# Kernel optimization log

Measured on AMD Instinct MI355X. Metric: run time of the kernel, lower is better.

The kernel has to match this reference:

```python
import jax, jax.numpy as jnp
import numpy as np
import math

B, S, D = 4, 1024, 1024
H, DK = 16, 64
NUM_BUCKETS = 32
MAX_DISTANCE = 128


def _relative_position_bucket(relative_position, bidirectional=True,
                              num_buckets=32, max_distance=128):
    # faithful port of T5's bucketing
    relative_buckets = jnp.zeros_like(relative_position)
    if bidirectional:
        num_buckets //= 2
        relative_buckets = relative_buckets + (relative_position > 0).astype(jnp.int32) * num_buckets
        relative_position = jnp.abs(relative_position)
    else:
        relative_position = -jnp.minimum(relative_position, jnp.zeros_like(relative_position))
    max_exact = num_buckets // 2
    is_small = relative_position < max_exact
    rp_safe = jnp.maximum(relative_position, 1)  # avoid log(0); masked by is_small
    rel_if_large = max_exact + (
        jnp.log(rp_safe.astype(jnp.float32) / max_exact)
        / math.log(max_distance / max_exact) * (num_buckets - max_exact)
    ).astype(jnp.int32)
    rel_if_large = jnp.minimum(rel_if_large, num_buckets - 1)
    return relative_buckets + jnp.where(is_small, relative_position, rel_if_large)


def compute_bias(rel_bias_emb, query_length, key_length):
    ctx = jnp.arange(query_length, dtype=jnp.int32)[:, None]
    mem = jnp.arange(key_length, dtype=jnp.int32)[None, :]
    rp = mem - ctx  # [q, k]
    buckets = _relative_position_bucket(rp, bidirectional=True,
                                        num_buckets=NUM_BUCKETS,
                                        max_distance=MAX_DISTANCE)
    values = rel_bias_emb[buckets]          # [q, k, h]
    return jnp.transpose(values, (2, 0, 1))[None]  # [1, h, q, k]


def setup_inputs() -> dict:
    key = jax.random.key(0)
    ks = jax.random.split(key, 6)
    s = 1.0 / math.sqrt(D)
    return {
        "hidden_states": jax.random.normal(ks[0], (B, S, D), jnp.float32),
        "Wq": jax.random.normal(ks[1], (D, H * DK), jnp.float32) * s,
        "Wk": jax.random.normal(ks[2], (D, H * DK), jnp.float32) * s,
        "Wv": jax.random.normal(ks[3], (D, H * DK), jnp.float32) * s,
        "Wo": jax.random.normal(ks[4], (H * DK, D), jnp.float32) * s,
        "rel_bias_emb": jax.random.normal(ks[5], (NUM_BUCKETS, H), jnp.float32),
    }


def reference(hidden_states, Wq, Wk, Wv, Wo, rel_bias_emb):
    b, s, _ = hidden_states.shape

    def shape_heads(x):  # [b, s, h*dk] -> [b, h, s, dk]
        return x.reshape(b, s, H, DK).transpose(0, 2, 1, 3)

    q = shape_heads(hidden_states @ Wq)
    k = shape_heads(hidden_states @ Wk)
    v = shape_heads(hidden_states @ Wv)

    # T5 attention: no 1/sqrt(dk) scaling
    scores = jnp.einsum('bhqd,bhkd->bhqk', q, k)
    position_bias = compute_bias(rel_bias_emb, s, s)  # [1, h, s, s]
    scores = scores + position_bias
    attn = jax.nn.softmax(scores.astype(jnp.float32), axis=-1).astype(scores.dtype)
    ctx = jnp.einsum('bhqk,bhkd->bhqd', attn, v)
    ctx = ctx.transpose(0, 2, 1, 3).reshape(b, s, H * DK)
    return ctx @ Wo
```

## Files before the change

### kernel.cpp

```cpp
#include <hip/hip_runtime.h>

typedef unsigned short u16;
typedef unsigned int u32;
typedef __bf16 bf16x8 __attribute__((ext_vector_type(8)));
typedef float f32x4 __attribute__((ext_vector_type(4)));

#define MFMA16(a, b, c) __builtin_amdgcn_mfma_f32_16x16x32_bf16(a, b, c, 0, 0, 0)
#define LOG2E 1.4426950408889634f

__device__ __forceinline__ u16 f2bf(float f) {
  u32 u = __float_as_uint(f);
  u += 0x7FFFu + ((u >> 16) & 1u);
  return (u16)(u >> 16);
}

__device__ __forceinline__ void gld16(u16* lds, const u16* g) {
  __builtin_amdgcn_global_load_lds((const __attribute__((address_space(1))) void*)g,
                                   (__attribute__((address_space(3))) void*)lds,
                                   16, 0, 0);
}

__device__ __forceinline__ int t5_bucket(int rp) {
  int ret = rp > 0 ? 16 : 0;
  int a = rp < 0 ? -rp : rp;
  int b;
  if      (a <  8) b = a;
  else if (a < 12) b = 8;
  else if (a < 16) b = 9;
  else if (a < 23) b = 10;
  else if (a < 32) b = 11;
  else if (a < 46) b = 12;
  else if (a < 64) b = 13;
  else if (a < 91) b = 14;
  else             b = 15;
  return ret + b;
}

__global__ __launch_bounds__(256) void prep(const float4* __restrict__ X, ushort4* __restrict__ Xb,
                                            const float* __restrict__ w0, const float* __restrict__ w1,
                                            const float* __restrict__ w2, const float* __restrict__ w3,
                                            u16* __restrict__ out) {
  int bid = blockIdx.x;
  if (bid < 512) {
#pragma unroll
    for (int i = 0; i < 8; i++) {
      int g = bid * 2048 + i * 256 + threadIdx.x;
      float4 v = X[g];
      ushort4 o;
      o.x = f2bf(v.x); o.y = f2bf(v.y); o.z = f2bf(v.z); o.w = f2bf(v.w);
      Xb[g] = o;
    }
    return;
  }
  bid -= 512;
  __shared__ __align__(16) u16 tb[64 * 68];
  const int col = threadIdx.x & 63;
  const int rowo = threadIdx.x >> 6;
#pragma unroll 1
  for (int t2 = 0; t2 < 2; t2++) {
    const int tile = bid * 2 + t2;
    const int z = tile >> 8, t = tile & 255;
    const float* W = (z == 0) ? w0 : (z == 1) ? w1 : (z == 2) ? w2 : w3;
    u16* O = out + z * 1048576;
    const int n0 = (t & 15) * 64, k0 = (t >> 4) * 64;
#pragma unroll
    for (int r = 0; r < 16; r++) {
      int kl = r * 4 + rowo;
      tb[col * 68 + kl] = f2bf(W[(k0 + kl) * 1024 + n0 + col]);
    }
    __syncthreads();
#pragma unroll
    for (int r = 0; r < 16; r++) {
      int nl = r * 4 + rowo;
      O[(n0 + nl) * 1024 + k0 + col] = tb[nl * 68 + col];
    }
    __syncthreads();
  }
}

__global__ __launch_bounds__(256) void gemm128(const u16* __restrict__ A,
                                               const u16* __restrict__ BtBase,
                                               u16* __restrict__ outp) {
  __shared__ __align__(16) u16 smem[24576];
  const int tid = threadIdx.x, lane = tid & 63, wave = tid >> 6;
  const int l15 = lane & 15, quad = lane >> 4;
  const int wm = (wave >> 1) * 64, wn = (wave & 1) * 64;

  const int id = blockIdx.x + blockIdx.y * 24;
  const int xcd = id & 7, jj = id >> 3;
  const int nz = (jj % 12) + (xcd & 1) * 12;
  const int ymb = (jj / 12) + (xcd >> 1) * 8;
  const int n = nz / 3, z = nz % 3;
  const int m0 = ymb * 128, n0 = n * 128;
  const u16* Ab = A + m0 * 1024;
  const u16* Bb = BtBase + z * 1048576 + n0 * 1024;

  int cc0 = tid, cc1 = 256 + tid;
  int row0 = cc0 >> 2, row1 = cc1 >> 2;
  int aoff0 = row0 * 1024 + (((cc0 & 3) ^ ((row0 >> 1) & 3)) * 8);
  int aoff1 = row1 * 1024 + (((cc1 & 3) ^ ((row1 >> 1) & 3)) * 8);

  f32x4 acc[4][4];
  const f32x4 vz = {0.f, 0.f, 0.f, 0.f};
#pragma unroll
  for (int i = 0; i < 4; i++)
#pragma unroll
    for (int j = 0; j < 4; j++) acc[i][j] = vz;

  const int sk = (l15 >> 1) & 3;

  {
    gld16(smem + cc0 * 8, Ab + aoff0);
    gld16(smem + cc1 * 8, Ab + aoff1);
    gld16(smem + 4096 + cc0 * 8, Bb + aoff0);
    gld16(smem + 4096 + cc1 * 8, Bb + aoff1);
    gld16(smem + 8192 + cc0 * 8, Ab + 32 + aoff0);
    gld16(smem + 8192 + cc1 * 8, Ab + 32 + aoff1);
    gld16(smem + 12288 + cc0 * 8, Bb + 32 + aoff0);
    gld16(smem + 12288 + cc1 * 8, Bb + 32 + aoff1);
  }

  int cs = 0, ls = 2;
#pragma unroll 1
  for (int kt = 0; kt < 32; kt++) {
    if (kt < 30) {
      u16* dst = smem + ls * 8192;
      const int ka = (kt + 2) * 32;
      gld16(dst + cc0 * 8, Ab + ka + aoff0);
      gld16(dst + cc1 * 8, Ab + ka + aoff1);
      gld16(dst + 4096 + cc0 * 8, Bb + ka + aoff0);
      gld16(dst + 4096 + cc1 * 8, Bb + ka + aoff1);
      asm volatile("s_waitcnt vmcnt(8)\n\ts_barrier" ::: "memory");
    } else if (kt == 30) {
      asm volatile("s_waitcnt vmcnt(4)\n\ts_barrier" ::: "memory");
    } else {
      asm volatile("s_waitcnt vmcnt(0)\n\ts_barrier" ::: "memory");
    }
    u16* st = smem + cs * 8192;
    bf16x8 af[4], bg[4];
#pragma unroll
    for (int mt = 0; mt < 4; mt++)
      af[mt] = *(const bf16x8*)(st + (wm + mt * 16 + l15) * 32 + ((quad ^ sk) * 8));
#pragma unroll
    for (int nt = 0; nt < 4; nt++)
      bg[nt] = *(const bf16x8*)(st + 4096 + (wn + nt * 16 + l15) * 32 + ((quad ^ sk) * 8));
#pragma unroll
    for (int mt = 0; mt < 4; mt++)
#pragma unroll
      for (int nt = 0; nt < 4; nt++)
        acc[mt][nt] = MFMA16(af[mt], bg[nt], acc[mt][nt]);
    asm volatile("s_barrier" ::: "memory");
    cs = (cs == 2) ? 0 : cs + 1;
    ls = (ls == 2) ? 0 : ls + 1;
  }
  __syncthreads();

  if (z == 2) {
    u16* O = outp + z * 4194304;
#pragma unroll
    for (int mt = 0; mt < 4; mt++)
#pragma unroll
      for (int nt = 0; nt < 4; nt++) {
        int col = wn + nt * 16 + l15;
        int rowb = wm + mt * 16 + quad * 4;
        uint2 p;
        p.x = (u32)f2bf(acc[mt][nt][0]) | ((u32)f2bf(acc[mt][nt][1]) << 16);
        p.y = (u32)f2bf(acc[mt][nt][2]) | ((u32)f2bf(acc[mt][nt][3]) << 16);
        *(uint2*)(smem + col * 136 + rowb) = p;
      }
    __syncthreads();
    const int b = m0 >> 10, sbase = m0 & 1023;
#pragma unroll
    for (int p = 0; p < 8; p++) {
      int g = p * 256 + tid;
      int col = g >> 4, chunk = g & 15;
      uint4 v = *(const uint4*)(smem + col * 136 + chunk * 8);
      int nn = n0 + col, hh = nn >> 6, dk = nn & 63;
      *(uint4*)(O + ((b * 16 + hh) * 64 + dk) * 1024 + sbase + chunk * 8) = v;
    }
  } else {
    u16* O = outp + z * 4194304;
    const float scl = (z == 0) ? LOG2E : 1.0f;
#pragma unroll
    for (int mt = 0; mt < 4; mt++)
#pragma unroll
      for (int nt = 0; nt < 4; nt++) {
        int rowb = wm + mt * 16 + quad * 4;
        int colb = wn + nt * 16 + l15;
#pragma unroll
        for (int reg = 0; reg < 4; reg++)
          smem[(rowb + reg) * 144 + colb] = f2bf(acc[mt][nt][reg] * scl);
      }
    __syncthreads();
    const int b = m0 >> 10, sbase = m0 & 1023;
#pragma unroll
    for (int p = 0; p < 8; p++) {
      int g = p * 256 + tid;
      int ml = g >> 4, c = g & 15;
      uint4 v = *(const uint4*)(smem + ml * 144 + c * 8);
      int nn = n0 + c * 8, hh = nn >> 6, dk = nn & 63;
      *(uint4*)(O + (b * 16 + hh) * 65536 + (sbase + ml) * 64 + dk) = v;
    }
  }
}

__global__ __launch_bounds__(256) void attn(const u16* __restrict__ Q, const u16* __restrict__ K,
                                            const u16* __restrict__ V, const float* __restrict__ emb,
                                            u16* __restrict__ ctx) {
  __shared__ __align__(16) u16 sKV[2 * 8192];
  __shared__ __align__(16) u16 sP[128 * 72];
  __shared__ __align__(16) float4 bt4[1156];
  const int tid = threadIdx.x, lane = tid & 63, wave = tid >> 6;
  const int l15 = lane & 15, quad = lane >> 4;
  const int bh = blockIdx.x, qt = blockIdx.y;
  const int h = bh & 15, b = bh >> 4;
  const u16* Qp = Q + bh * 65536 + qt * 8192;
  const u16* Kp = K + bh * 65536;
  const u16* Vp = V + bh * 65536;
  const int sx = l15 & 7;

  int koff[2], voff[2], cbs[2];
#pragma unroll
  for (int r = 0; r < 2; r++) {
    int cb = r * 256 + wave * 64;
    int cc = cb + lane;
    int row = cc >> 3, c8 = (cc & 7) ^ (row & 7);
    koff[r] = row * 64 + c8 * 8;
    voff[r] = row * 1024 + c8 * 8;
    cbs[r] = cb * 8;
  }

  bf16x8 aq[2][2];
#pragma unroll
  for (int u = 0; u < 2; u++)
#pragma unroll
    for (int kk = 0; kk < 2; kk++)
      aq[u][kk] = *(const bf16x8*)(Qp + (wave * 32 + u * 16 + l15) * 64 + kk * 32 + quad * 8);

#pragma unroll
  for (int r = 0; r < 2; r++) {
    gld16(sKV + cbs[r], Kp + koff[r]);
    gld16(sKV + 4096 + cbs[r], Vp + voff[r]);
  }

  for (int i = tid; i < 1156; i += 256) {
    int rp0 = i - 127 - qt * 128;
    float4 v;
    v.x = emb[t5_bucket(rp0)     * 16 + h] * LOG2E;
    v.y = emb[t5_bucket(rp0 + 1) * 16 + h] * LOG2E;
    v.z = emb[t5_bucket(rp0 + 2) * 16 + h] * LOG2E;
    v.w = emb[t5_bucket(rp0 + 3) * 16 + h] * LOG2E;
    bt4[i] = v;
  }
  const float bias_pos = emb[31 * 16 + h] * LOG2E;
  const float bias_neg = emb[15 * 16 + h] * LOG2E;

  float2 ls2[2] = {{0.f, 0.f}, {0.f, 0.f}};
  f32x4 oc[2][4];
  const f32x4 vzero = {0.f, 0.f, 0.f, 0.f};
#pragma unroll
  for (int u = 0; u < 2; u++)
#pragma unroll
    for (int nt = 0; nt < 4; nt++) oc[u][nt] = vzero;

  __syncthreads();

#pragma unroll 1
  for (int j = 0; j < 16; j++) {
    u16* st = sKV + (j & 1) * 8192;
    if (j < 15) {
      u16* dst = sKV + ((j + 1) & 1) * 8192;
      const u16* Kj1 = Kp + (j + 1) * 4096;
      const u16* Vj1 = Vp + (j + 1) * 64;
#pragma unroll
      for (int r = 0; r < 2; r++) {
        gld16(dst + cbs[r], Kj1 + koff[r]);
        gld16(dst + 4096 + cbs[r], Vj1 + voff[r]);
      }
      asm volatile("s_waitcnt vmcnt(4)\n\ts_barrier" ::: "memory");
    } else {
      asm volatile("s_waitcnt vmcnt(0)\n\ts_barrier" ::: "memory");
    }

    f32x4 sc[4][2];
    const int rp_min = j * 64 - qt * 128 - 127;
    const int rp_max = j * 64 + 63 - qt * 128;
    if (rp_min >= 91) {
#pragma unroll
      for (int mt = 0; mt < 4; mt++)
#pragma unroll
        for (int u = 0; u < 2; u++) { sc[mt][u][0] = bias_pos; sc[mt][u][1] = bias_pos; sc[mt][u][2] = bias_pos; sc[mt][u][3] = bias_pos; }
    } else if (rp_max <= -91) {
#pragma unroll
      for (int mt = 0; mt < 4; mt++)
#pragma unroll
        for (int u = 0; u < 2; u++) { sc[mt][u][0] = bias_neg; sc[mt][u][1] = bias_neg; sc[mt][u][2] = bias_neg; sc[mt][u][3] = bias_neg; }
    } else {
#pragma unroll
      for (int mt = 0; mt < 4; mt++)
#pragma unroll
        for (int u = 0; u < 2; u++) {
          int idx = j * 64 + mt * 16 + quad * 4 - wave * 32 - u * 16 - l15 + 127;
          float4 bv4 = bt4[idx];
          sc[mt][u][0] = bv4.x; sc[mt][u][1] = bv4.y; sc[mt][u][2] = bv4.z; sc[mt][u][3] = bv4.w;
        }
    }
#pragma unroll
    for (int kk = 0; kk < 2; kk++) {
      bf16x8 ak[4];
      int g8 = kk * 4 + quad;
#pragma unroll
      for (int mt = 0; mt < 4; mt++)
        ak[mt] = *(const bf16x8*)(st + (mt * 16 + l15) * 64 + (g8 ^ sx) * 8);
#pragma unroll
      for (int mt = 0; mt < 4; mt++)
#pragma unroll
        for (int u = 0; u < 2; u++)
          sc[mt][u] = MFMA16(ak[mt], aq[u][kk], sc[mt][u]);
    }

#pragma unroll
    for (int u = 0; u < 2; u++) {
      const int prow = wave * 32 + u * 16 + l15;
#pragma unroll
      for (int mt = 0; mt < 4; mt++) {
        u32 b0 = __float_as_uint(__builtin_amdgcn_exp2f(sc[mt][u][0]));
        u32 b1 = __float_as_uint(__builtin_amdgcn_exp2f(sc[mt][u][1]));
        u32 b2 = __float_as_uint(__builtin_amdgcn_exp2f(sc[mt][u][2]));
        u32 b3 = __float_as_uint(__builtin_amdgcn_exp2f(sc[mt][u][3]));
        u32 t0 = b0 & 0xFFFF0000u, t1 = b1 & 0xFFFF0000u;
        u32 t2 = b2 & 0xFFFF0000u, t3 = b3 & 0xFFFF0000u;
        ls2[u].x += __uint_as_float(t0) + __uint_as_float(t2);
        ls2[u].y += __uint_as_float(t1) + __uint_as_float(t3);
        uint2 pk;
        pk.x = (t0 >> 16) | t1;
        pk.y = (t2 >> 16) | t3;
        *(uint2*)(sP + prow * 72 + mt * 16 + quad * 4) = pk;
      }
    }
    asm volatile("s_waitcnt lgkmcnt(0)" ::: "memory");

#pragma unroll
    for (int kk = 0; kk < 2; kk++) {
      bf16x8 ap[2];
      int g8 = kk * 4 + quad;
#pragma unroll
      for (int u = 0; u < 2; u++)
        ap[u] = *(const bf16x8*)(sP + (wave * 32 + u * 16 + l15) * 72 + kk * 32 + quad * 8);
#pragma unroll
      for (int nt = 0; nt < 4; nt++) {
        bf16x8 bv = *(const bf16x8*)(st + 4096 + (nt * 16 + l15) * 64 + (g8 ^ sx) * 8);
#pragma unroll
        for (int u = 0; u < 2; u++)
          oc[u][nt] = MFMA16(ap[u], bv, oc[u][nt]);
      }
    }
    asm volatile("s_barrier" ::: "memory");
  }

  float lsum[2];
#pragma unroll
  for (int u = 0; u < 2; u++) {
    lsum[u] = ls2[u].x + ls2[u].y;
    lsum[u] += __shfl_xor(lsum[u], 16, 64);
    lsum[u] += __shfl_xor(lsum[u], 32, 64);
  }
  float linv[2][4];
#pragma unroll
  for (int u = 0; u < 2; u++)
#pragma unroll
    for (int reg = 0; reg < 4; reg++)
      linv[u][reg] = __builtin_amdgcn_rcpf(__shfl(lsum[u], quad * 4 + reg, 64));

  u16* cb2 = ctx + b * 1048576 + (qt * 128 + wave * 32) * 1024 + h * 64;
#pragma unroll
  for (int u = 0; u < 2; u++)
#pragma unroll
    for (int nt = 0; nt < 4; nt++)
#pragma unroll
      for (int reg = 0; reg < 4; reg++)
        cb2[(u * 16 + quad * 4 + reg) * 1024 + nt * 16 + l15] = f2bf(oc[u][nt][reg] * linv[u][reg]);
}

__global__ __launch_bounds__(256) void gemm_o(const u16* __restrict__ A,
                                              const u16* __restrict__ Bt,
                                              float* __restrict__ O) {
  __shared__ __align__(16) u16 smem[36864];
  const int tid = threadIdx.x, lane = tid & 63, wave = tid >> 6;
  const int l15 = lane & 15, quad = lane >> 4;
  const int m0 = blockIdx.x * 64, n0 = blockIdx.y * 128;
  const u16* Ab = A + m0 * 1024;
  const u16* Bb = Bt + n0 * 1024;
  const int wn = wave * 32;

  int ar0 = tid >> 3, ar1 = (256 + tid) >> 3;
  int aoff0 = ar0 * 1024 + (((tid & 7) ^ (ar0 & 7)) * 8);
  int aoff1 = ar1 * 1024 + ((((256 + tid) & 7) ^ (ar1 & 7)) * 8);
  int boff[4], bdst[4];
#pragma unroll
  for (int r = 0; r < 4; r++) {
    int cc = r * 256 + tid;
    int row = cc >> 3;
    boff[r] = row * 1024 + (((cc & 7) ^ (row & 7)) * 8);
    bdst[r] = cc * 8;
  }

  f32x4 acc[4][2];
  const f32x4 vz = {0.f, 0.f, 0.f, 0.f};
#pragma unroll
  for (int i = 0; i < 4; i++) { acc[i][0] = vz; acc[i][1] = vz; }

  const int sx = l15 & 7;

#pragma unroll
  for (int s = 0; s < 2; s++) {
    u16* st = smem + s * 12288;
    const int ka = s * 64;
    gld16(st + tid * 8, Ab + ka + aoff0);
    gld16(st + (256 + tid) * 8, Ab + ka + aoff1);
#pragma unroll
    for (int r = 0; r < 4; r++) gld16(st + 4096 + bdst[r], Bb + ka + boff[r]);
  }

  int cs = 0, ls = 2;
#pragma unroll 1
  for (int kt = 0; kt < 16; kt++) {
    if (kt < 14) {
      u16* dst = smem + ls * 12288;
      const int ka = (kt + 2) * 64;
      gld16(dst + tid * 8, Ab + ka + aoff0);
      gld16(dst + (256 + tid) * 8, Ab + ka + aoff1);
#pragma unroll
      for (int r = 0; r < 4; r++) gld16(dst + 4096 + bdst[r], Bb + ka + boff[r]);
      asm volatile("s_waitcnt vmcnt(12)\n\ts_barrier" ::: "memory");
    } else if (kt == 14) {
      asm volatile("s_waitcnt vmcnt(6)\n\ts_barrier" ::: "memory");
    } else {
      asm volatile("s_waitcnt vmcnt(0)\n\ts_barrier" ::: "memory");
    }
    u16* st = smem + cs * 12288;
#pragma unroll
    for (int kk = 0; kk < 2; kk++) {
      bf16x8 af[4], bg[2];
      int g8 = kk * 4 + quad;
#pragma unroll
      for (int mt = 0; mt < 4; mt++)
        af[mt] = *(const bf16x8*)(st + (mt * 16 + l15) * 64 + ((g8 ^ sx) * 8));
#pragma unroll
      for (int nt = 0; nt < 2; nt++)
        bg[nt] = *(const bf16x8*)(st + 4096 + (wn + nt * 16 + l15) * 64 + ((g8 ^ sx) * 8));
#pragma unroll
      for (int mt = 0; mt < 4; mt++)
#pragma unroll
        for (int nt = 0; nt < 2; nt++)
          acc[mt][nt] = MFMA16(af[mt], bg[nt], acc[mt][nt]);
    }
    asm volatile("s_barrier" ::: "memory");
    cs = (cs == 2) ? 0 : cs + 1;
    ls = (ls == 2) ? 0 : ls + 1;
  }

#pragma unroll
  for (int mt = 0; mt < 4; mt++)
#pragma unroll
    for (int nt = 0; nt < 2; nt++)
#pragma unroll
      for (int reg = 0; reg < 4; reg++) {
        int row = m0 + mt * 16 + quad * 4 + reg;
        int col = n0 + wn + nt * 16 + l15;
        O[row * 1024 + col] = acc[mt][nt][reg];
      }
}

extern "C" void kernel_launch(void* const* d_in, const int* in_sizes, int n_in,
                              void* d_out, int out_size, void* d_ws, size_t ws_size,
                              hipStream_t stream) {
  (void)in_sizes; (void)n_in; (void)out_size; (void)ws_size;
  const float* X   = (const float*)d_in[0];
  const float* Wq  = (const float*)d_in[1];
  const float* Wk  = (const float*)d_in[2];
  const float* Wv  = (const float*)d_in[3];
  const float* Wo  = (const float*)d_in[4];
  const float* emb = (const float*)d_in[5];

  char* ws = (char*)d_ws;
  u16* Xb  = (u16*)(ws);
  u16* Wt  = (u16*)(ws + (8u  << 20));
  u16* Qb  = (u16*)(ws + (16u << 20));
  u16* Ctx = (u16*)(ws + (40u << 20));

  prep<<<1024, 256, 0, stream>>>((const float4*)X, (ushort4*)Xb, Wq, Wk, Wv, Wo, Wt);
  gemm128<<<dim3(24, 32), 256, 0, stream>>>(Xb, Wt, Qb);
  attn<<<dim3(64, 8), 256, 0, stream>>>(Qb, Qb + 4194304, Qb + 2 * 4194304, emb, Ctx);
  gemm_o<<<dim3(64, 8), 256, 0, stream>>>(Ctx, Wt + 3 * 1048576, (float*)d_out);
}
```

Baseline: 163.7 us.

## Split QKV projection into 128x256 Q/K kernel and separate V GEMM, enlarge output-GEMM tile

Replaces the single fused QKV GEMM (128x128 tiles with an XCD-aware remap) with a 512-thread kernel that computes Q and K using 128x256 tiles, plus a separate GEMM for V that keeps its transposed store. The output projection moves from 64x128 to 128x128 tiles with four 64x64 waves, so operand tiles are reused more per block. In exchange it adds a kernel launch, drops the XCD grouping, and lowers block counts, which reduces occupancy and parallelism on a 256-CU device.

After: 172.5 us. +5.4%, slower.

```diff
diff --git a/kernel.cpp b/kernel.cpp
--- a/kernel.cpp
+++ b/kernel.cpp
@@ -78,22 +78,120 @@
   }
 }
 
-__global__ __launch_bounds__(256) void gemm128(const u16* __restrict__ A,
-                                               const u16* __restrict__ BtBase,
-                                               u16* __restrict__ outp) {
+__global__ __launch_bounds__(512) void qk512(const u16* __restrict__ A,
+                                             const u16* __restrict__ Wt,
+                                             u16* __restrict__ outp) {
+  __shared__ __align__(16) u16 smem[36864];
+  const int tid = threadIdx.x, lane = tid & 63, wave = tid >> 6;
+  const int l15 = lane & 15, quad = (lane >> 4) & 3;
+  const int wm = (wave >> 2) * 64, wn = (wave & 3) * 64;
+  const int id = blockIdx.x;
+  const int nq = id & 7, m = id >> 3;
+  const int m0 = m * 128, n0 = nq * 256;
+  const int z = nq >> 2;
+  const u16* Ab = A + m0 * 1024;
+  const u16* Bb = Wt + n0 * 1024;
+
+  const int ar = tid >> 2;
+  const int aoff = ar * 1024 + (((tid & 3) ^ ((ar >> 1) & 3)) * 8);
+  int boff[2], bdst[2];
+#pragma unroll
+  for (int r = 0; r < 2; r++) {
+    int cc = r * 512 + tid;
+    int row = cc >> 2;
+    boff[r] = row * 1024 + (((cc & 3) ^ ((row >> 1) & 3)) * 8);
+    bdst[r] = 4096 + cc * 8;
+  }
+
+  f32x4 acc[4][4];
+  const f32x4 vz = {0.f, 0.f, 0.f, 0.f};
+#pragma unroll
+  for (int i = 0; i < 4; i++)
+#pragma unroll
+    for (int j = 0; j < 4; j++) acc[i][j] = vz;
+
+  const int sk = (l15 >> 1) & 3;
+
+#pragma unroll
+  for (int s = 0; s < 2; s++) {
+    u16* st = smem + s * 12288;
+    const int ka = s * 32;
+    gld16(st + tid * 8, Ab + ka + aoff);
+    gld16(st + bdst[0], Bb + ka + boff[0]);
+    gld16(st + bdst[1], Bb + ka + boff[1]);
+  }
+
+  int cs = 0, ls = 2;
+#pragma unroll 1
+  for (int kt = 0; kt < 32; kt++) {
+    if (kt < 30) {
+      u16* dst = smem + ls * 12288;
+      const int ka = (kt + 2) * 32;
+      gld16(dst + tid * 8, Ab + ka + aoff);
+      gld16(dst + bdst[0], Bb + ka + boff[0]);
+      gld16(dst + bdst[1], Bb + ka + boff[1]);
+      asm volatile("s_waitcnt vmcnt(6)\n\ts_barrier" ::: "memory");
+    } else if (kt == 30) {
+      asm volatile("s_waitcnt vmcnt(3)\n\ts_barrier" ::: "memory");
+    } else {
+      asm volatile("s_waitcnt vmcnt(0)\n\ts_barrier" ::: "memory");
+    }
+    u16* st = smem + cs * 12288;
+    bf16x8 af[4], bg[4];
+#pragma unroll
+    for (int mt = 0; mt < 4; mt++)
+      af[mt] = *(const bf16x8*)(st + (wm + mt * 16 + l15) * 32 + ((quad ^ sk) * 8));
+#pragma unroll
+    for (int nt = 0; nt < 4; nt++)
+      bg[nt] = *(const bf16x8*)(st + 4096 + (wn + nt * 16 + l15) * 32 + ((quad ^ sk) * 8));
+#pragma unroll
+    for (int mt = 0; mt < 4; mt++)
+#pragma unroll
+      for (int nt = 0; nt < 4; nt++)
+        acc[mt][nt] = MFMA16(af[mt], bg[nt], acc[mt][nt]);
+    asm volatile("s_barrier" ::: "memory");
+    cs = (cs == 2) ? 0 : cs + 1;
+    ls = (ls == 2) ? 0 : ls + 1;
+  }
+  __syncthreads();
+
+  const float scl = (z == 0) ? LOG2E : 1.0f;
+#pragma unroll
+  for (int mt = 0; mt < 4; mt++)
+#pragma unroll
+    for (int nt = 0; nt < 4; nt++) {
+      int rowb = wm + mt * 16 + quad * 4;
+      int colb = wn + nt * 16 + l15;
+#pragma unroll
+      for (int reg = 0; reg < 4; reg++)
+        smem[(rowb + reg) * 264 + colb] = f2bf(acc[mt][nt][reg] * scl);
+    }
+  __syncthreads();
+  u16* O = outp + z * 4194304;
+  const int b = m0 >> 10, sbase = m0 & 1023;
+#pragma unroll
+  for (int p = 0; p < 8; p++) {
+    int g = p * 512 + tid;
+    int ml = g >> 5, c = g & 31;
+    uint4 v = *(const uint4*)(smem + ml * 264 + c * 8);
+    int col10 = (n0 & 1023) + c * 8;
+    int hh = col10 >> 6, dk = col10 & 63;
+    *(uint4*)(O + (b * 16 + hh) * 65536 + (sbase + ml) * 64 + dk) = v;
+  }
+}
+
+__global__ __launch_bounds__(256) void gemmv(const u16* __restrict__ A,
+                                             const u16* __restrict__ Bt,
+                                             u16* __restrict__ Vt) {
   __shared__ __align__(16) u16 smem[24576];
   const int tid = threadIdx.x, lane = tid & 63, wave = tid >> 6;
   const int l15 = lane & 15, quad = lane >> 4;
   const int wm = (wave >> 1) * 64, wn = (wave & 1) * 64;
-
-  const int id = blockIdx.x + blockIdx.y * 24;
-  const int xcd = id & 7, jj = id >> 3;
-  const int nz = (jj % 12) + (xcd & 1) * 12;
-  const int ymb = (jj / 12) + (xcd >> 1) * 8;
-  const int n = nz / 3, z = nz % 3;
-  const int m0 = ymb * 128, n0 = n * 128;
+  const int id = blockIdx.x + blockIdx.y * 8;
+  const int n = id & 7, m = id >> 3;
+  const int m0 = m * 128, n0 = n * 128;
   const u16* Ab = A + m0 * 1024;
-  const u16* Bb = BtBase + z * 1048576 + n0 * 1024;
+  const u16* Bb = Bt + n0 * 1024;
 
   int cc0 = tid, cc1 = 256 + tid;
   int row0 = cc0 >> 2, row1 = cc1 >> 2;
@@ -109,15 +207,14 @@
 
   const int sk = (l15 >> 1) & 3;
 
-  {
-    gld16(smem + cc0 * 8, Ab + aoff0);
-    gld16(smem + cc1 * 8, Ab + aoff1);
-    gld16(smem + 4096 + cc0 * 8, Bb + aoff0);
-    gld16(smem + 4096 + cc1 * 8, Bb + aoff1);
-    gld16(smem + 8192 + cc0 * 8, Ab + 32 + aoff0);
-    gld16(smem + 8192 + cc1 * 8, Ab + 32 + aoff1);
-    gld16(smem + 12288 + cc0 * 8, Bb + 32 + aoff0);
-    gld16(smem + 12288 + cc1 * 8, Bb + 32 + aoff1);
+#pragma unroll
+  for (int s = 0; s < 2; s++) {
+    u16* st = smem + s * 8192;
+    const int ka = s * 32;
+    gld16(st + cc0 * 8, Ab + ka + aoff0);
+    gld16(st + cc1 * 8, Ab + ka + aoff1);
+    gld16(st + 4096 + cc0 * 8, Bb + ka + aoff0);
+    gld16(st + 4096 + cc1 * 8, Bb + ka + aoff1);
   }
 
   int cs = 0, ls = 2;
@@ -155,52 +252,26 @@
   }
   __syncthreads();
 
-  if (z == 2) {
-    u16* O = outp + z * 4194304;
-#pragma unroll
-    for (int mt = 0; mt < 4; mt++)
-#pragma unroll
-      for (int nt = 0; nt < 4; nt++) {
-        int col = wn + nt * 16 + l15;
-        int rowb = wm + mt * 16 + quad * 4;
-        uint2 p;
-        p.x = (u32)f2bf(acc[mt][nt][0]) | ((u32)f2bf(acc[mt][nt][1]) << 16);
-        p.y = (u32)f2bf(acc[mt][nt][2]) | ((u32)f2bf(acc[mt][nt][3]) << 16);
-        *(uint2*)(smem + col * 136 + rowb) = p;
-      }
-    __syncthreads();
-    const int b = m0 >> 10, sbase = m0 & 1023;
-#pragma unroll
-    for (int p = 0; p < 8; p++) {
-      int g = p * 256 + tid;
-      int col = g >> 4, chunk = g & 15;
-      uint4 v = *(const uint4*)(smem + col * 136 + chunk * 8);
-      int nn = n0 + col, hh = nn >> 6, dk = nn & 63;
-      *(uint4*)(O + ((b * 16 + hh) * 64 + dk) * 1024 + sbase + chunk * 8) = v;
-    }
-  } else {
-    u16* O = outp + z * 4194304;
-    const float scl = (z == 0) ? LOG2E : 1.0f;
-#pragma unroll
-    for (int mt = 0; mt < 4; mt++)
-#pragma unroll
-      for (int nt = 0; nt < 4; nt++) {
-        int rowb = wm + mt * 16 + quad * 4;
-        int colb = wn + nt * 16 + l15;
-#pragma unroll
-        for (int reg = 0; reg < 4; reg++)
-          smem[(rowb + reg) * 144 + colb] = f2bf(acc[mt][nt][reg] * scl);
-      }
-    __syncthreads();
-    const int b = m0 >> 10, sbase = m0 & 1023;
-#pragma unroll
-    for (int p = 0; p < 8; p++) {
-      int g = p * 256 + tid;
-      int ml = g >> 4, c = g & 15;
-      uint4 v = *(const uint4*)(smem + ml * 144 + c * 8);
-      int nn = n0 + c * 8, hh = nn >> 6, dk = nn & 63;
-      *(uint4*)(O + (b * 16 + hh) * 65536 + (sbase + ml) * 64 + dk) = v;
-    }
+#pragma unroll
+  for (int mt = 0; mt < 4; mt++)
+#pragma unroll
+    for (int nt = 0; nt < 4; nt++) {
+      int col = wn + nt * 16 + l15;
+      int rowb = wm + mt * 16 + quad * 4;
+      uint2 p;
+      p.x = (u32)f2bf(acc[mt][nt][0]) | ((u32)f2bf(acc[mt][nt][1]) << 16);
+      p.y = (u32)f2bf(acc[mt][nt][2]) | ((u32)f2bf(acc[mt][nt][3]) << 16);
+      *(uint2*)(smem + col * 136 + rowb) = p;
+    }
+  __syncthreads();
+  const int b = m0 >> 10, sbase = m0 & 1023;
+#pragma unroll
+  for (int p = 0; p < 8; p++) {
+    int g = p * 256 + tid;
+    int col = g >> 4, chunk = g & 15;
+    uint4 v = *(const uint4*)(smem + col * 136 + chunk * 8);
+    int nn = n0 + col, hh = nn >> 6, dk = nn & 63;
+    *(uint4*)(Vt + ((b * 16 + hh) * 64 + dk) * 1024 + sbase + chunk * 8) = v;
   }
 }
 
@@ -385,74 +456,77 @@
 __global__ __launch_bounds__(256) void gemm_o(const u16* __restrict__ A,
                                               const u16* __restrict__ Bt,
                                               float* __restrict__ O) {
-  __shared__ __align__(16) u16 smem[36864];
+  __shared__ __align__(16) u16 smem[49152];
   const int tid = threadIdx.x, lane = tid & 63, wave = tid >> 6;
   const int l15 = lane & 15, quad = lane >> 4;
-  const int m0 = blockIdx.x * 64, n0 = blockIdx.y * 128;
+  const int wm = (wave >> 1) * 64, wn = (wave & 1) * 64;
+  const int id = blockIdx.x + blockIdx.y * 8;
+  const int n = id & 7, m = id >> 3;
+  const int m0 = m * 128, n0 = n * 128;
   const u16* Ab = A + m0 * 1024;
   const u16* Bb = Bt + n0 * 1024;
-  const int wn = wave * 32;
-
-  int ar0 = tid >> 3, ar1 = (256 + tid) >> 3;
-  int aoff0 = ar0 * 1024 + (((tid & 7) ^ (ar0 & 7)) * 8);
-  int aoff1 = ar1 * 1024 + ((((256 + tid) & 7) ^ (ar1 & 7)) * 8);
-  int boff[4], bdst[4];
+
+  int soff[4], sdst[4];
 #pragma unroll
   for (int r = 0; r < 4; r++) {
     int cc = r * 256 + tid;
     int row = cc >> 3;
-    boff[r] = row * 1024 + (((cc & 7) ^ (row & 7)) * 8);
-    bdst[r] = cc * 8;
-  }
-
-  f32x4 acc[4][2];
+    soff[r] = row * 1024 + (((cc & 7) ^ (row & 7)) * 8);
+    sdst[r] = cc * 8;
+  }
+
+  f32x4 acc[4][4];
   const f32x4 vz = {0.f, 0.f, 0.f, 0.f};
 #pragma unroll
-  for (int i = 0; i < 4; i++) { acc[i][0] = vz; acc[i][1] = vz; }
+  for (int i = 0; i < 4; i++)
+#pragma unroll
+    for (int j = 0; j < 4; j++) acc[i][j] = vz;
 
   const int sx = l15 & 7;
 
 #pragma unroll
   for (int s = 0; s < 2; s++) {
-    u16* st = smem + s * 12288;
+    u16* st = smem + s * 16384;
     const int ka = s * 64;
-    gld16(st + tid * 8, Ab + ka + aoff0);
-    gld16(st + (256 + tid) * 8, Ab + ka + aoff1);
-#pragma unroll
-    for (int r = 0; r < 4; r++) gld16(st + 4096 + bdst[r], Bb + ka + boff[r]);
+#pragma unroll
+    for (int r = 0; r < 4; r++) {
+      gld16(st + sdst[r], Ab + ka + soff[r]);
+      gld16(st + 8192 + sdst[r], Bb + ka + soff[r]);
+    }
   }
 
   int cs = 0, ls = 2;
 #pragma unroll 1
   for (int kt = 0; kt < 16; kt++) {
     if (kt < 14) {
-      u16* dst = smem + ls * 12288;
+      u16* dst = smem + ls * 16384;
       const int ka = (kt + 2) * 64;
-      gld16(dst + tid * 8, Ab + ka + aoff0);
-      gld16(dst + (256 + tid) * 8, Ab + ka + aoff1);
-#pragma unroll
-      for (int r = 0; r < 4; r++) gld16(dst + 4096 + bdst[r], Bb + ka + boff[r]);
-      asm volatile("s_waitcnt vmcnt(12)\n\ts_barrier" ::: "memory");
+#pragma unroll
+      for (int r = 0; r < 4; r++) {
+        gld16(dst + sdst[r], Ab + ka + soff[r]);
+        gld16(dst + 8192 + sdst[r], Bb + ka + soff[r]);
+      }
+      asm volatile("s_waitcnt vmcnt(16)\n\ts_barrier" ::: "memory");
     } else if (kt == 14) {
-      asm volatile("s_waitcnt vmcnt(6)\n\ts_barrier" ::: "memory");
+      asm volatile("s_waitcnt vmcnt(8)\n\ts_barrier" ::: "memory");
     } else {
       asm volatile("s_waitcnt vmcnt(0)\n\ts_barrier" ::: "memory");
     }
-    u16* st = smem + cs * 12288;
+    u16* st = smem + cs * 16384;
 #pragma unroll
     for (int kk = 0; kk < 2; kk++) {
-      bf16x8 af[4], bg[2];
+      bf16x8 af[4], bg[4];
       int g8 = kk * 4 + quad;
 #pragma unroll
       for (int mt = 0; mt < 4; mt++)
-        af[mt] = *(const bf16x8*)(st + (mt * 16 + l15) * 64 + ((g8 ^ sx) * 8));
-#pragma unroll
-      for (int nt = 0; nt < 2; nt++)
-        bg[nt] = *(const bf16x8*)(st + 4096 + (wn + nt * 16 + l15) * 64 + ((g8 ^ sx) * 8));
-#pragma unroll
-      for (int mt = 0; mt < 4; mt++)
-#pragma unroll
-        for (int nt = 0; nt < 2; nt++)
+        af[mt] = *(const bf16x8*)(st + (wm + mt * 16 + l15) * 64 + ((g8 ^ sx) * 8));
+#pragma unroll
+      for (int nt = 0; nt < 4; nt++)
+        bg[nt] = *(const bf16x8*)(st + 8192 + (wn + nt * 16 + l15) * 64 + ((g8 ^ sx) * 8));
+#pragma unroll
+      for (int mt = 0; mt < 4; mt++)
+#pragma unroll
+        for (int nt = 0; nt < 4; nt++)
           acc[mt][nt] = MFMA16(af[mt], bg[nt], acc[mt][nt]);
     }
     asm volatile("s_barrier" ::: "memory");
@@ -463,10 +537,10 @@
 #pragma unroll
   for (int mt = 0; mt < 4; mt++)
 #pragma unroll
-    for (int nt = 0; nt < 2; nt++)
+    for (int nt = 0; nt < 4; nt++)
 #pragma unroll
       for (int reg = 0; reg < 4; reg++) {
-        int row = m0 + mt * 16 + quad * 4 + reg;
+        int row = m0 + wm + mt * 16 + quad * 4 + reg;
         int col = n0 + wn + nt * 16 + l15;
         O[row * 1024 + col] = acc[mt][nt][reg];
       }
@@ -490,7 +564,8 @@
   u16* Ctx = (u16*)(ws + (40u << 20));
 
   prep<<<1024, 256, 0, stream>>>((const float4*)X, (ushort4*)Xb, Wq, Wk, Wv, Wo, Wt);
-  gemm128<<<dim3(24, 32), 256, 0, stream>>>(Xb, Wt, Qb);
+  qk512<<<256, 512, 0, stream>>>(Xb, Wt, Qb);
+  gemmv<<<dim3(8, 32), 256, 0, stream>>>(Xb, Wt + 2 * 1048576, Qb + 2 * 4194304);
   attn<<<dim3(64, 8), 256, 0, stream>>>(Qb, Qb + 4194304, Qb + 2 * 4194304, emb, Ctx);
-  gemm_o<<<dim3(64, 8), 256, 0, stream>>>(Ctx, Wt + 3 * 1048576, (float*)d_out);
-}
+  gemm_o<<<dim3(8, 32), 256, 0, stream>>>(Ctx, Wt + 3 * 1048576, (float*)d_out);
+}
```
